# Optimization experiments

Measured on AMD Instinct MI355X. Metric: run time of the kernel, lower is better.

Reference implementation:

```python
import jax, jax.numpy as jnp
import numpy as np

OBS, ACT, EMB, HID, NQ = 512, 32, 512, 512, 32
B = 32768


def setup_inputs() -> dict:
    key = jax.random.key(0)
    ks = jax.random.split(key, 12)
    s_in = 1.0 / np.sqrt(OBS + ACT)
    s_emb = 1.0 / np.sqrt(EMB)
    s_hid = 1.0 / np.sqrt(HID)
    return {
        "observation": jax.random.normal(ks[0], (B, OBS), jnp.float32),
        "prev_action": jax.random.normal(ks[1], (B, ACT), jnp.float32),
        "hidden_state": jax.random.normal(ks[2], (HID,), jnp.float32),
        "cell_state": jax.random.normal(ks[3], (HID,), jnp.float32),
        "W1": jax.random.uniform(ks[4], (EMB, OBS + ACT), jnp.float32, -s_in, s_in),
        "b1": jax.random.uniform(ks[5], (EMB,), jnp.float32, -s_in, s_in),
        "W_ih": jax.random.uniform(ks[6], (4 * HID, EMB), jnp.float32, -s_hid, s_hid),
        "b_ih": jax.random.uniform(ks[7], (4 * HID,), jnp.float32, -s_hid, s_hid),
        "W_hh": jax.random.uniform(ks[8], (4 * HID, HID), jnp.float32, -s_hid, s_hid),
        "b_hh": jax.random.uniform(ks[9], (4 * HID,), jnp.float32, -s_hid, s_hid),
        "W2": jax.random.uniform(ks[10], (NQ, HID), jnp.float32, -s_hid, s_hid),
        "b2": jax.random.uniform(ks[11], (NQ,), jnp.float32, -s_hid, s_hid),
    }


def reference(observation, prev_action, hidden_state, cell_state,
              W1, b1, W_ih, b_ih, W_hh, b_hh, W2, b2):
    # MLP1: Linear + ReLU over concat(obs, prev_action)  -> [B, EMB]
    x = jnp.concatenate([observation, prev_action], axis=-1)
    x = jax.nn.relu(x @ W1.T + b1)

    # Original torch code loops LSTMCell over batch, but reuses the SAME
    # (hidden_state, cell_state) every iteration -> fully batchable.
    # gates: [B, 4H]; h contribution is identical for all rows (broadcast).
    gates = x @ W_ih.T + b_ih + (hidden_state @ W_hh.T + b_hh)
    i, f, g, o = jnp.split(gates, 4, axis=-1)  # torch LSTMCell gate order
    i = jax.nn.sigmoid(i)
    f = jax.nn.sigmoid(f)
    g = jnp.tanh(g)
    o = jax.nn.sigmoid(o)
    c_new = f * cell_state + i * g          # [B, HID]
    h_new = o * jnp.tanh(c_new)             # [B, HID]

    q_values = h_new @ W2.T + b2             # [B, NQ]
    # torch returns last loop iteration's (h, c)
    return q_values, h_new[-1], c_new[-1]
```

## Files before the change

### kernel.cpp

```cpp
#include <hip/hip_runtime.h>
#include <stdint.h>

#define DEVINL __device__ __forceinline__

typedef __attribute__((ext_vector_type(8))) __bf16 bf16x8;
typedef __attribute__((ext_vector_type(4))) float f32x4;
typedef __attribute__((ext_vector_type(16))) float f32x16;
typedef __attribute__((ext_vector_type(4))) int i32x4;
typedef __attribute__((ext_vector_type(8))) int i32x8;

DEVINL unsigned short f2bf(float f) {
  union { float f; unsigned int u; } v; v.f = f;
  unsigned int u = v.u;
  return (unsigned short)((u + 0x7fffu + ((u >> 16) & 1u)) >> 16);
}

DEVINL unsigned char f2fp8(float f) {
  return (unsigned char)(__builtin_amdgcn_cvt_pk_fp8_f32(f, f, 0, false) & 0xff);
}

DEVINL float sigm(float x) { return __builtin_amdgcn_rcpf(1.f + __expf(-x)); }
DEVINL float tanh_(float x) {
  return 1.f - 2.f * __builtin_amdgcn_rcpf(1.f + __expf(2.f * x));
}

#define GLD_LDS16(gptr, lptr)                                                  \
  __builtin_amdgcn_global_load_lds(                                            \
      (__attribute__((address_space(1))) void*)(gptr),                         \
      (__attribute__((address_space(3))) void*)(lptr), 16, 0, 0)

#define TOPBAR_4 asm volatile("s_waitcnt vmcnt(4) lgkmcnt(0)\n\ts_barrier" ::: "memory")
#define TOPBAR_1 asm volatile("s_waitcnt vmcnt(1) lgkmcnt(0)\n\ts_barrier" ::: "memory")
#define TOPBAR_0 asm volatile("s_waitcnt vmcnt(0) lgkmcnt(0)\n\ts_barrier" ::: "memory")
#define BOTBAR   asm volatile("s_waitcnt lgkmcnt(0)\n\ts_barrier" ::: "memory")

DEVINL int swz_col(int c) { return ((c & 3) ^ ((c >> 3) & 3)) * 8; }
DEVINL int swz16(int c) { return ((c & 3) ^ ((c >> 3) & 3)) * 16; }

__global__ void prep_all(const float* __restrict__ obs, const float* __restrict__ act,
                         const float* __restrict__ W1, const float* __restrict__ Wih,
                         const float* __restrict__ W2, const float* __restrict__ Whh,
                         const float* __restrict__ hid, const float* __restrict__ bhh,
                         const float* __restrict__ bih,
                         unsigned short* __restrict__ A0, unsigned short* __restrict__ W1b,
                         unsigned char* __restrict__ Wih8, unsigned short* __restrict__ W2b,
                         float* __restrict__ hvec) {
  const int bid = blockIdx.x, tid = threadIdx.x;
  if (bid < 2176) {
    const int total = 32768 * 68;
    for (int c = bid * 256 + tid; c < total; c += 2176 * 256) {
      const int b = c / 68, c8 = c % 68;
      const float* src = (c8 < 64) ? (obs + (size_t)b * 512 + c8 * 8)
                                   : (act + (size_t)b * 32 + (c8 - 64) * 8);
      float4 f0 = *(const float4*)src;
      float4 f1 = *(const float4*)(src + 4);
      unsigned short u[8] = {f2bf(f0.x), f2bf(f0.y), f2bf(f0.z), f2bf(f0.w),
                             f2bf(f1.x), f2bf(f1.y), f2bf(f1.z), f2bf(f1.w)};
      *(uint4*)(A0 + (size_t)b * 544 + c8 * 8) = *(uint4*)u;
    }
  } else if (bid < 2176 + 1312) {
    const int i = (bid - 2176) * 256 + tid;
    if (i < 69632) {
      float4 f = *(const float4*)(W1 + (size_t)i * 4);
      unsigned short u[4] = {f2bf(f.x), f2bf(f.y), f2bf(f.z), f2bf(f.w)};
      *(uint2*)(W1b + (size_t)i * 4) = *(uint2*)u;
    } else if (i < 69632 + 262144) {
      const int off = i - 69632;
      const int row = off >> 7, col0 = (off & 127) * 4;
      float4 f = *(const float4*)(Wih + (size_t)off * 4);
      int pk = __builtin_amdgcn_cvt_pk_fp8_f32(f.x * 16.f, f.y * 16.f, 0, false);
      pk = __builtin_amdgcn_cvt_pk_fp8_f32(f.z * 16.f, f.w * 16.f, pk, true);
      *(unsigned int*)(Wih8 + (size_t)row * 512 + col0) = (unsigned int)pk;
    } else {
      const int off = i - 331776;
      float4 f = *(const float4*)(W2 + (size_t)off * 4);
      unsigned short u[4] = {f2bf(f.x), f2bf(f.y), f2bf(f.z), f2bf(f.w)};
      *(uint2*)(W2b + (size_t)off * 4) = *(uint2*)u;
    }
  } else {
    const int j = (bid - 3488) * 4 + (tid >> 6);
    const int lane = tid & 63;
    const float* w = Whh + (size_t)j * 512;
    float s = 0.f;
    for (int k = lane; k < 512; k += 64) s += w[k] * hid[k];
    for (int off = 32; off; off >>= 1) s += __shfl_down(s, off, 64);
    if (lane == 0) hvec[j] = s + bhh[j] + bih[j];
  }
}

__global__ __launch_bounds__(256, 2) void gemm1_relu(
    const unsigned short* __restrict__ A0,
    const unsigned short* __restrict__ W1b,
    const float* __restrict__ b1,
    unsigned char* __restrict__ X8) {
  constexpr int KT = 17, LD = 544;
  __shared__ __align__(16) unsigned short As[2][128 * 32];
  __shared__ __align__(16) unsigned short Bs[2][128 * 32];
  const int tid = threadIdx.x, wave = tid >> 6, lane = tid & 63;
  const int id = blockIdx.x, xcd = id & 7, slot = id >> 3;
  const int m0 = (xcd * 32 + (slot >> 2)) * 128;
  const int n0 = (slot & 3) * 128;
  const int wr = (wave >> 1) * 64, wc = (wave & 1) * 64;
  f32x4 acc[4][4] = {};

  const int c0 = tid, c1 = tid + 256;
  const unsigned short* pA0 = A0 + (size_t)(m0 + (c0 >> 2)) * LD + swz_col(c0);
  const unsigned short* pA1 = A0 + (size_t)(m0 + (c1 >> 2)) * LD + swz_col(c1);
  const unsigned short* pB0 = W1b + (size_t)(n0 + (c0 >> 2)) * LD + swz_col(c0);
  const unsigned short* pB1 = W1b + (size_t)(n0 + (c1 >> 2)) * LD + swz_col(c1);
  const int fr = lane & 15, q = lane >> 4;
  const int koff = (q ^ ((fr >> 1) & 3)) * 8;

#define STAGE1(buf)                                                            \
  do {                                                                         \
    GLD_LDS16(pA0, &As[(buf)][wave * 512]);                                    \
    GLD_LDS16(pA1, &As[(buf)][2048 + wave * 512]);                             \
    GLD_LDS16(pB0, &Bs[(buf)][wave * 512]);                                    \
    GLD_LDS16(pB1, &Bs[(buf)][2048 + wave * 512]);                             \
    pA0 += 32; pA1 += 32; pB0 += 32; pB1 += 32;                                \
  } while (0)

  STAGE1(0);
  for (int kt = 0; kt < KT; ++kt) {
    if (kt + 1 < KT) { STAGE1((kt + 1) & 1); TOPBAR_4; } else { TOPBAR_0; }
    const unsigned short* as = As[kt & 1];
    const unsigned short* bs = Bs[kt & 1];
    bf16x8 a[4], b[4];
#pragma unroll
    for (int i = 0; i < 4; ++i) a[i] = *(const bf16x8*)&as[(wr + i * 16 + fr) * 32 + koff];
#pragma unroll
    for (int j = 0; j < 4; ++j) b[j] = *(const bf16x8*)&bs[(wc + j * 16 + fr) * 32 + koff];
#pragma unroll
    for (int i = 0; i < 4; ++i)
#pragma unroll
      for (int j = 0; j < 4; ++j)
        acc[i][j] = __builtin_amdgcn_mfma_f32_16x16x32_bf16(a[i], b[j], acc[i][j], 0, 0, 0);
    BOTBAR;
  }
#undef STAGE1
  const int rbase = q * 4, cn = fr;
#pragma unroll
  for (int i = 0; i < 4; ++i)
#pragma unroll
    for (int j = 0; j < 4; ++j) {
      const int gn = n0 + wc + j * 16 + cn;
      const float bias = b1[gn];
#pragma unroll
      for (int r = 0; r < 4; ++r) {
        const int gm = m0 + wr + i * 16 + rbase + r;
        float v = acc[i][j][r] + bias;
        v = v > 0.f ? v : 0.f;
        X8[(size_t)gm * 512 + gn] = f2fp8(v * 8.f);
      }
    }
}

__global__ __launch_bounds__(256, 3) void gemm2_lstm(
    const unsigned char* __restrict__ X8,
    const unsigned char* __restrict__ Wih8,
    const float* __restrict__ hvec,
    const float* __restrict__ cell,
    unsigned short* __restrict__ H,
    float* __restrict__ hlast,
    float* __restrict__ clast) {
  constexpr int KT = 8;
  __shared__ __align__(16) unsigned char As[2][128 * 64];
  __shared__ __align__(16) unsigned char Bs[2][4 * 32 * 64];
  const int tid = threadIdx.x, wave = tid >> 6, lane = tid & 63;
  const int id = blockIdx.x, xcd = id & 7, slot = id >> 3;
  const int m0 = (xcd * 32 + (slot >> 4)) * 128;
  const int n0 = (slot & 15) * 32;
  f32x16 acc[4] = {};

  const int c0 = tid, c1 = tid + 256;
  const unsigned char* pA0 = X8 + (size_t)(m0 + (c0 >> 2)) * 512 + swz16(c0);
  const unsigned char* pA1 = X8 + (size_t)(m0 + (c1 >> 2)) * 512 + swz16(c1);
  const unsigned char* pB0 =
      Wih8 + (size_t)((c0 >> 7) * 512 + n0 + ((c0 >> 2) & 31)) * 512 + swz16(c0);
  const unsigned char* pB1 =
      Wih8 + (size_t)((c1 >> 7) * 512 + n0 + ((c1 >> 2) & 31)) * 512 + swz16(c1);

  const int r31 = lane & 31, g2 = lane >> 5;
  const int sw = (r31 >> 1) & 3;
  const int plo = ((2 * g2) ^ sw) * 16, phi = ((2 * g2 + 1) ^ sw) * 16;
  const int arow = (wave * 32 + r31) * 64;
  const int brow = r31 * 64;

#define STAGE2(buf)                                                            \
  do {                                                                         \
    GLD_LDS16(pA0, &As[(buf)][wave * 1024]);                                   \
    GLD_LDS16(pA1, &As[(buf)][4096 + wave * 1024]);                            \
    GLD_LDS16(pB0, &Bs[(buf)][wave * 1024]);                                   \
    GLD_LDS16(pB1, &Bs[(buf)][4096 + wave * 1024]);                            \
    pA0 += 64; pA1 += 64; pB0 += 64; pB1 += 64;                                \
  } while (0)

  STAGE2(0);
  for (int kt = 0; kt < KT; ++kt) {
    if (kt + 1 < KT) { STAGE2((kt + 1) & 1); TOPBAR_4; } else { TOPBAR_0; }
    const unsigned char* as = As[kt & 1];
    const unsigned char* bs = Bs[kt & 1];
    i32x4 alo = *(const i32x4*)&as[arow + plo];
    i32x4 ahi = *(const i32x4*)&as[arow + phi];
    i32x8 a = __builtin_shufflevector(alo, ahi, 0, 1, 2, 3, 4, 5, 6, 7);
    i32x8 b[4];
#pragma unroll
    for (int qd = 0; qd < 4; ++qd) {
      i32x4 blo = *(const i32x4*)&bs[qd * 2048 + brow + plo];
      i32x4 bhi = *(const i32x4*)&bs[qd * 2048 + brow + phi];
      b[qd] = __builtin_shufflevector(blo, bhi, 0, 1, 2, 3, 4, 5, 6, 7);
    }
#pragma unroll
    for (int qd = 0; qd < 4; ++qd)
      acc[qd] = __builtin_amdgcn_mfma_scale_f32_32x32x64_f8f6f4(
          a, b[qd], acc[qd],
          0, 0,
          0, 0x7f7f7f7f,
          0, 0x7f7f7f7f);
    BOTBAR;
  }
#undef STAGE2

  const int gn = n0 + r31;
  const float hv_i = hvec[gn];
  const float hv_f = hvec[gn + 512];
  const float hv_g = hvec[gn + 1024];
  const float hv_o = hvec[gn + 1536];
  const float cprev = cell[gn];
  constexpr float S = 1.f / 128.f;
#pragma unroll
  for (int rg = 0; rg < 4; ++rg)
#pragma unroll
    for (int rr = 0; rr < 4; ++rr) {
      const int reg = rg * 4 + rr;
      const int gm = m0 + wave * 32 + rr + rg * 8 + g2 * 4;
      float si = sigm(acc[0][reg] * S + hv_i);
      float sf = sigm(acc[1][reg] * S + hv_f);
      float tg = tanh_(acc[2][reg] * S + hv_g);
      float so = sigm(acc[3][reg] * S + hv_o);
      float cnew = sf * cprev + si * tg;
      float hnew = so * tanh_(cnew);
      H[(size_t)gm * 512 + gn] = f2bf(hnew);
      if (gm == 32767) { hlast[gn] = hnew; clast[gn] = cnew; }
    }
}

__global__ __launch_bounds__(256, 2) void gemm3(
    const unsigned short* __restrict__ H,
    const unsigned short* __restrict__ W2b,
    const float* __restrict__ b2,
    float* __restrict__ Q) {
  constexpr int KT = 16, LDW = 520;
  __shared__ __align__(16) unsigned short As[2][64 * 32];
  __shared__ __align__(16) unsigned short Ws[32 * LDW];
  const int tid = threadIdx.x, wave = tid >> 6, lane = tid & 63;
  const int id = blockIdx.x;
  const int m0 = ((id & 7) * 64 + (id >> 3)) * 64;
  for (int c = tid; c < 2048; c += 256) {
    const int row = c >> 6, col8 = c & 63;
    *(uint4*)&Ws[row * LDW + col8 * 8] = *(const uint4*)(W2b + row * 512 + col8 * 8);
  }
  f32x4 acc[2] = {};
  const int c0 = tid;
  const unsigned short* pA0 = H + (size_t)(m0 + (c0 >> 2)) * 512 + swz_col(c0);
  const int fr = lane & 15, q = lane >> 4;
  const int koff = (q ^ ((fr >> 1) & 3)) * 8;

#define STAGE3(buf)                                                            \
  do {                                                                         \
    GLD_LDS16(pA0, &As[(buf)][wave * 512]);                                    \
    pA0 += 32;                                                                 \
  } while (0)

  STAGE3(0);
  for (int kt = 0; kt < KT; ++kt) {
    if (kt + 1 < KT) { STAGE3((kt + 1) & 1); TOPBAR_1; } else { TOPBAR_0; }
    const unsigned short* as = As[kt & 1];
    const int k0 = kt * 32;
    bf16x8 a  = *(const bf16x8*)&as[(wave * 16 + fr) * 32 + koff];
    bf16x8 b0 = *(const bf16x8*)&Ws[fr * LDW + k0 + q * 8];
    bf16x8 b1 = *(const bf16x8*)&Ws[(16 + fr) * LDW + k0 + q * 8];
    acc[0] = __builtin_amdgcn_mfma_f32_16x16x32_bf16(a, b0, acc[0], 0, 0, 0);
    acc[1] = __builtin_amdgcn_mfma_f32_16x16x32_bf16(a, b1, acc[1], 0, 0, 0);
    BOTBAR;
  }
#undef STAGE3
  const int rbase = q * 4;
#pragma unroll
  for (int j = 0; j < 2; ++j) {
    const int gn = j * 16 + fr;
    const float bias = b2[gn];
#pragma unroll
    for (int r = 0; r < 4; ++r) {
      const int gm = m0 + wave * 16 + rbase + r;
      Q[(size_t)gm * 32 + gn] = acc[j][r] + bias;
    }
  }
}

extern "C" void kernel_launch(void* const* d_in, const int* in_sizes, int n_in,
                              void* d_out, int out_size, void* d_ws, size_t ws_size,
                              hipStream_t stream) {
  const float* obs  = (const float*)d_in[0];
  const float* act  = (const float*)d_in[1];
  const float* hid  = (const float*)d_in[2];
  const float* cell = (const float*)d_in[3];
  const float* W1   = (const float*)d_in[4];
  const float* b1   = (const float*)d_in[5];
  const float* Wih  = (const float*)d_in[6];
  const float* bih  = (const float*)d_in[7];
  const float* Whh  = (const float*)d_in[8];
  const float* bhh  = (const float*)d_in[9];
  const float* W2   = (const float*)d_in[10];
  const float* b2   = (const float*)d_in[11];
  float* out = (float*)d_out;

  char* ws = (char*)d_ws;
  unsigned short* A0   = (unsigned short*)(ws);
  unsigned short* H    = (unsigned short*)(ws);
  unsigned char*  X8   = (unsigned char*)(ws + 35651584);
  unsigned short* W1b  = (unsigned short*)(ws + 52428800);
  unsigned char*  Wih8 = (unsigned char*)(ws + 52985856);
  unsigned short* W2b  = (unsigned short*)(ws + 54034432);
  float*          hvec = (float*)(ws + 54067200);

  prep_all<<<4000, 256, 0, stream>>>(obs, act, W1, Wih, W2, Whh, hid, bhh, bih,
                                     A0, W1b, Wih8, W2b, hvec);
  gemm1_relu<<<1024, 256, 0, stream>>>(A0, W1b, b1, X8);
  gemm2_lstm<<<4096, 256, 0, stream>>>(X8, Wih8, hvec, cell, H,
                                       out + 32768 * 32,
                                       out + 32768 * 32 + 512);
  gemm3<<<512, 256, 0, stream>>>(H, W2b, b2, out);
}
```

Before: 216.5 us.

## Double gemm2 M-tile to 256 rows and load LDS in MFMA-native fragment order

The LSTM gate GEMM now gives each block 256 rows instead of 128. Each wave computes two 32-row fragments against the four gate tiles, so every B fragment read from LDS is reused twice and Wih is refetched from memory half as often. Global-to-LDS loads are rearranged so each lane's 16-byte chunk lands where the MFMA read expects it, replacing the XOR swizzle with a linear lane*16 layout. In exchange the block uses more LDS and accumulator registers, occupancy drops from 3 to 2 blocks, the grid halves, and the linear layout may bring LDS bank conflicts.

```diff
diff --git a/kernel.cpp b/kernel.cpp
--- a/kernel.cpp
+++ b/kernel.cpp
@@ -29,13 +29,13 @@
       (__attribute__((address_space(1))) void*)(gptr),                         \
       (__attribute__((address_space(3))) void*)(lptr), 16, 0, 0)
 
+#define TOPBAR_6 asm volatile("s_waitcnt vmcnt(6) lgkmcnt(0)\n\ts_barrier" ::: "memory")
 #define TOPBAR_4 asm volatile("s_waitcnt vmcnt(4) lgkmcnt(0)\n\ts_barrier" ::: "memory")
 #define TOPBAR_1 asm volatile("s_waitcnt vmcnt(1) lgkmcnt(0)\n\ts_barrier" ::: "memory")
 #define TOPBAR_0 asm volatile("s_waitcnt vmcnt(0) lgkmcnt(0)\n\ts_barrier" ::: "memory")
 #define BOTBAR   asm volatile("s_waitcnt lgkmcnt(0)\n\ts_barrier" ::: "memory")
 
 DEVINL int swz_col(int c) { return ((c & 3) ^ ((c >> 3) & 3)) * 8; }
-DEVINL int swz16(int c) { return ((c & 3) ^ ((c >> 3) & 3)) * 16; }
 
 __global__ void prep_all(const float* __restrict__ obs, const float* __restrict__ act,
                          const float* __restrict__ W1, const float* __restrict__ Wih,
@@ -155,7 +155,7 @@
     }
 }
 
-__global__ __launch_bounds__(256, 3) void gemm2_lstm(
+__global__ __launch_bounds__(256, 2) void gemm2_lstm(
     const unsigned char* __restrict__ X8,
     const unsigned char* __restrict__ Wih8,
     const float* __restrict__ hvec,
@@ -164,59 +164,67 @@
     float* __restrict__ hlast,
     float* __restrict__ clast) {
   constexpr int KT = 8;
-  __shared__ __align__(16) unsigned char As[2][128 * 64];
+  __shared__ __align__(16) unsigned char As[2][256 * 64];
   __shared__ __align__(16) unsigned char Bs[2][4 * 32 * 64];
   const int tid = threadIdx.x, wave = tid >> 6, lane = tid & 63;
   const int id = blockIdx.x, xcd = id & 7, slot = id >> 3;
-  const int m0 = (xcd * 32 + (slot >> 4)) * 128;
+  const int m0 = (xcd * 16 + (slot >> 4)) * 256;
   const int n0 = (slot & 15) * 32;
-  f32x16 acc[4] = {};
-
-  const int c0 = tid, c1 = tid + 256;
-  const unsigned char* pA0 = X8 + (size_t)(m0 + (c0 >> 2)) * 512 + swz16(c0);
-  const unsigned char* pA1 = X8 + (size_t)(m0 + (c1 >> 2)) * 512 + swz16(c1);
+  f32x16 acc00 = {}, acc01 = {}, acc02 = {}, acc03 = {};
+  f32x16 acc10 = {}, acc11 = {}, acc12 = {}, acc13 = {};
+
+  const int r31 = lane & 31, g2 = lane >> 5;
+  const int fA = wave >> 1, hA = wave & 1;
+  const size_t acol = (size_t)(g2 * 32 + hA * 16);
+  const unsigned char* pA0 = X8 + (size_t)(m0 + 0 * 64 + fA * 32 + r31) * 512 + acol;
+  const unsigned char* pA1 = X8 + (size_t)(m0 + 1 * 64 + fA * 32 + r31) * 512 + acol;
+  const unsigned char* pA2 = X8 + (size_t)(m0 + 2 * 64 + fA * 32 + r31) * 512 + acol;
+  const unsigned char* pA3 = X8 + (size_t)(m0 + 3 * 64 + fA * 32 + r31) * 512 + acol;
   const unsigned char* pB0 =
-      Wih8 + (size_t)((c0 >> 7) * 512 + n0 + ((c0 >> 2) & 31)) * 512 + swz16(c0);
+      Wih8 + (size_t)((0 + fA) * 512 + n0 + r31) * 512 + acol;
   const unsigned char* pB1 =
-      Wih8 + (size_t)((c1 >> 7) * 512 + n0 + ((c1 >> 2) & 31)) * 512 + swz16(c1);
-
-  const int r31 = lane & 31, g2 = lane >> 5;
-  const int sw = (r31 >> 1) & 3;
-  const int plo = ((2 * g2) ^ sw) * 16, phi = ((2 * g2 + 1) ^ sw) * 16;
-  const int arow = (wave * 32 + r31) * 64;
-  const int brow = r31 * 64;
+      Wih8 + (size_t)((2 + fA) * 512 + n0 + r31) * 512 + acol;
+
+  const int lb = lane * 16;
 
 #define STAGE2(buf)                                                            \
   do {                                                                         \
     GLD_LDS16(pA0, &As[(buf)][wave * 1024]);                                   \
     GLD_LDS16(pA1, &As[(buf)][4096 + wave * 1024]);                            \
+    GLD_LDS16(pA2, &As[(buf)][8192 + wave * 1024]);                            \
+    GLD_LDS16(pA3, &As[(buf)][12288 + wave * 1024]);                           \
     GLD_LDS16(pB0, &Bs[(buf)][wave * 1024]);                                   \
     GLD_LDS16(pB1, &Bs[(buf)][4096 + wave * 1024]);                            \
-    pA0 += 64; pA1 += 64; pB0 += 64; pB1 += 64;                                \
+    pA0 += 64; pA1 += 64; pA2 += 64; pA3 += 64; pB0 += 64; pB1 += 64;          \
   } while (0)
+
+#define LDPAIR(dst, base_ptr, off)                                             \
+  do {                                                                         \
+    i32x4 lo_ = *(const i32x4*)((base_ptr) + (off) + lb);                      \
+    i32x4 hi_ = *(const i32x4*)((base_ptr) + (off) + 1024 + lb);               \
+    dst = __builtin_shufflevector(lo_, hi_, 0, 1, 2, 3, 4, 5, 6, 7);           \
+  } while (0)
+
+#define MFMA_MX(acc_, a_, b_)                                                  \
+  acc_ = __builtin_amdgcn_mfma_scale_f32_32x32x64_f8f6f4(                      \
+      a_, b_, acc_, 0, 0, 0, 0x7f7f7f7f, 0, 0x7f7f7f7f)
 
   STAGE2(0);
   for (int kt = 0; kt < KT; ++kt) {
-    if (kt + 1 < KT) { STAGE2((kt + 1) & 1); TOPBAR_4; } else { TOPBAR_0; }
+    if (kt + 1 < KT) { STAGE2((kt + 1) & 1); TOPBAR_6; } else { TOPBAR_0; }
     const unsigned char* as = As[kt & 1];
     const unsigned char* bs = Bs[kt & 1];
-    i32x4 alo = *(const i32x4*)&as[arow + plo];
-    i32x4 ahi = *(const i32x4*)&as[arow + phi];
-    i32x8 a = __builtin_shufflevector(alo, ahi, 0, 1, 2, 3, 4, 5, 6, 7);
-    i32x8 b[4];
-#pragma unroll
-    for (int qd = 0; qd < 4; ++qd) {
-      i32x4 blo = *(const i32x4*)&bs[qd * 2048 + brow + plo];
-      i32x4 bhi = *(const i32x4*)&bs[qd * 2048 + brow + phi];
-      b[qd] = __builtin_shufflevector(blo, bhi, 0, 1, 2, 3, 4, 5, 6, 7);
-    }
-#pragma unroll
-    for (int qd = 0; qd < 4; ++qd)
-      acc[qd] = __builtin_amdgcn_mfma_scale_f32_32x32x64_f8f6f4(
-          a, b[qd], acc[qd],
-          0, 0,
-          0, 0x7f7f7f7f,
-          0, 0x7f7f7f7f);
+    i32x8 b0, b1, b2, b3, a0, a1;
+    LDPAIR(b0, bs, 0);
+    LDPAIR(b1, bs, 2048);
+    LDPAIR(b2, bs, 4096);
+    LDPAIR(b3, bs, 6144);
+    LDPAIR(a0, as, wave * 4096);
+    LDPAIR(a1, as, wave * 4096 + 2048);
+    MFMA_MX(acc00, a0, b0); MFMA_MX(acc01, a0, b1);
+    MFMA_MX(acc02, a0, b2); MFMA_MX(acc03, a0, b3);
+    MFMA_MX(acc10, a1, b0); MFMA_MX(acc11, a1, b1);
+    MFMA_MX(acc12, a1, b2); MFMA_MX(acc13, a1, b3);
     BOTBAR;
   }
 #undef STAGE2
@@ -228,21 +236,30 @@
   const float hv_o = hvec[gn + 1536];
   const float cprev = cell[gn];
   constexpr float S = 1.f / 128.f;
-#pragma unroll
-  for (int rg = 0; rg < 4; ++rg)
-#pragma unroll
-    for (int rr = 0; rr < 4; ++rr) {
-      const int reg = rg * 4 + rr;
-      const int gm = m0 + wave * 32 + rr + rg * 8 + g2 * 4;
-      float si = sigm(acc[0][reg] * S + hv_i);
-      float sf = sigm(acc[1][reg] * S + hv_f);
-      float tg = tanh_(acc[2][reg] * S + hv_g);
-      float so = sigm(acc[3][reg] * S + hv_o);
-      float cnew = sf * cprev + si * tg;
-      float hnew = so * tanh_(cnew);
-      H[(size_t)gm * 512 + gn] = f2bf(hnew);
-      if (gm == 32767) { hlast[gn] = hnew; clast[gn] = cnew; }
-    }
+
+#define EPILOG(F, ai, af, ag, ao)                                              \
+  _Pragma("unroll")                                                            \
+  for (int rg = 0; rg < 4; ++rg) {                                             \
+    _Pragma("unroll")                                                          \
+    for (int rr = 0; rr < 4; ++rr) {                                           \
+      const int reg = rg * 4 + rr;                                             \
+      const int gm = m0 + wave * 64 + (F) * 32 + rr + rg * 8 + g2 * 4;         \
+      float si = sigm(ai[reg] * S + hv_i);                                     \
+      float sf = sigm(af[reg] * S + hv_f);                                     \
+      float tg = tanh_(ag[reg] * S + hv_g);                                    \
+      float so = sigm(ao[reg] * S + hv_o);                                     \
+      float cnew = sf * cprev + si * tg;                                       \
+      float hnew = so * tanh_(cnew);                                           \
+      H[(size_t)gm * 512 + gn] = f2bf(hnew);                                   \
+      if (gm == 32767) { hlast[gn] = hnew; clast[gn] = cnew; }                 \
+    }                                                                          \
+  }
+
+  EPILOG(0, acc00, acc01, acc02, acc03)
+  EPILOG(1, acc10, acc11, acc12, acc13)
+#undef EPILOG
+#undef LDPAIR
+#undef MFMA_MX
 }
 
 __global__ __launch_bounds__(256, 2) void gemm3(
@@ -327,7 +344,7 @@
   prep_all<<<4000, 256, 0, stream>>>(obs, act, W1, Wih, W2, Whh, hid, bhh, bih,
                                      A0, W1b, Wih8, W2b, hvec);
   gemm1_relu<<<1024, 256, 0, stream>>>(A0, W1b, b1, X8);
-  gemm2_lstm<<<4096, 256, 0, stream>>>(X8, Wih8, hvec, cell, H,
+  gemm2_lstm<<<2048, 256, 0, stream>>>(X8, Wih8, hvec, cell, H,
                                        out + 32768 * 32,
                                        out + 32768 * 32 + 512);
   gemm3<<<512, 256, 0, stream>>>(H, W2b, b2, out);
```

After: 230.0 us. +6.2%, slower.
